# Kernel tuning notes

Hardware: AMD Instinct MI355X
Metric: run time of the kernel (lower is better)

## Reference

```python
import jax, jax.numpy as jnp
import numpy as np

N = 50000      # nodes
E = 800000     # edges
D_IN = 512
H = 256        # hidden_dim


def setup_inputs() -> dict:
    key = jax.random.key(0)
    ks = jax.random.split(key, 16)
    def w(k, shape):
        fan_in = shape[0]
        return (jax.random.normal(k, shape, jnp.float32) / np.sqrt(fan_in)).astype(jnp.float32)
    return {
        "x": jax.random.normal(ks[0], (N, D_IN), jnp.float32),
        "edge_index": jax.random.randint(ks[1], (2, E), 0, N),
        "W1": w(ks[2], (D_IN, H)),      "b1": jnp.zeros((H,), jnp.float32),
        "W2": w(ks[3], (H, H)),          "b2": jnp.zeros((H,), jnp.float32),
        "W3": w(ks[4], (H, H // 2)),     "b3": jnp.zeros((H // 2,), jnp.float32),
        "We": w(ks[5], (H // 2, 3)),     "be": jnp.zeros((3,), jnp.float32),
        "Wh": w(ks[6], (H // 2, 3)),     "bh": jnp.zeros((3,), jnp.float32),
        "Wg": w(ks[7], (H // 2, 3)),     "bg": jnp.zeros((3,), jnp.float32),
    }


def _gcn(h, W, b, src, dst, norm_edge, norm_self):
    # GCNConv: X' = D^{-1/2} (A + I) D^{-1/2} X W + b  (lin first, then aggregate)
    h = h @ W                                             # [N, out]
    msg = h[src] * norm_edge[:, None]                     # [E, out]
    agg = jax.ops.segment_sum(msg, dst, num_segments=N)   # neighbor sum
    agg = agg + h * norm_self[:, None]                    # self-loop term
    return agg + b


def reference(x, edge_index, W1, b1, W2, b2, W3, b3, We, be, Wh, bh, Wg, bg):
    src, dst = edge_index[0], edge_index[1]
    # degree of A + I (unit edge weights + self loop)
    deg = jax.ops.segment_sum(jnp.ones((E,), jnp.float32), dst, num_segments=N) + 1.0
    dinv = jax.lax.rsqrt(deg)
    norm_edge = dinv[src] * dinv[dst]   # [E]
    norm_self = dinv * dinv             # [N]

    h1 = jax.nn.relu(_gcn(x,  W1, b1, src, dst, norm_edge, norm_self))
    h2 = jax.nn.relu(_gcn(h1, W2, b2, src, dst, norm_edge, norm_self))
    h3 = jax.nn.relu(_gcn(h2, W3, b3, src, dst, norm_edge, norm_self))

    emp = h3 @ We + be
    hc  = h3 @ Wh + bh
    gro = h3 @ Wg + bg
    return jnp.concatenate([emp, hc, gro], axis=1)  # [N, 9]
```

## Files before the change

kernel.cpp:

```cpp
#include <hip/hip_runtime.h>

#define N_NODES 50000
#define N_EDGES 800000
#define MP 50048

typedef __attribute__((ext_vector_type(8))) short bf16x8;
typedef __attribute__((ext_vector_type(4))) float f32x4;
typedef _Float16 f16;
typedef __attribute__((ext_vector_type(4))) _Float16 half4;
typedef __attribute__((ext_vector_type(2))) _Float16 half2v;

__device__ __forceinline__ unsigned short f2bf(float f) {
    unsigned u = __float_as_uint(f);
    u += 0x7fffu + ((u >> 16) & 1u);
    return (unsigned short)(u >> 16);
}
__device__ __forceinline__ float bf2f(unsigned short h) {
    return __uint_as_float(((unsigned)h) << 16);
}


__global__ void hist_kernel(const int* __restrict__ dst, int* __restrict__ deg, int e) {
    int i = blockIdx.x * blockDim.x + threadIdx.x;
    if (i < e) atomicAdd(&deg[dst[i]], 1);
}

__global__ void dinv_kernel(const int* __restrict__ deg, float* __restrict__ dinv, int n) {
    int i = blockIdx.x * blockDim.x + threadIdx.x;
    if (i < n) dinv[i] = rsqrtf((float)deg[i] + 1.0f);
}

__global__ __launch_bounds__(1024) void scan_kernel(const int* __restrict__ counts,
                                                    int* __restrict__ row_start, int n) {
    __shared__ int wsum[16];
    __shared__ int carry_s;
    int tid = threadIdx.x, wid = tid >> 6, lane = tid & 63;
    if (tid == 0) carry_s = 0;
    __syncthreads();
    for (int base = 0; base < n; base += 1024) {
        int i = base + tid;
        int v = (i < n) ? counts[i] : 0;
        int s = v;
        #pragma unroll
        for (int off = 1; off < 64; off <<= 1) {
            int t = __shfl_up(s, off, 64);
            if (lane >= off) s += t;
        }
        if (lane == 63) wsum[wid] = s;
        __syncthreads();
        if (wid == 0) {
            int ws = (lane < 16) ? wsum[lane] : 0;
            #pragma unroll
            for (int off = 1; off < 16; off <<= 1) {
                int t = __shfl_up(ws, off, 64);
                if (lane >= off) ws += t;
            }
            if (lane < 16) wsum[lane] = ws;
        }
        __syncthreads();
        int carry = carry_s;
        if (i < n) row_start[i] = carry + ((wid == 0) ? 0 : wsum[wid - 1]) + s - v;
        int total = wsum[15];
        __syncthreads();
        if (tid == 0) carry_s = carry + total;
        __syncthreads();
    }
    if (tid == 0) row_start[n] = carry_s;
}

__global__ void scatter_kernel(const int* __restrict__ src, const int* __restrict__ dst,
                               const float* __restrict__ dinv,
                               const int* __restrict__ row_start, int* __restrict__ cursor,
                               int* __restrict__ csr_src, float* __restrict__ csr_w, int e) {
    int i = blockIdx.x * blockDim.x + threadIdx.x;
    if (i < e) {
        int d = dst[i], s = src[i];
        int p = atomicAdd(&cursor[d], 1);
        int idx = row_start[d] + p;
        csr_src[idx] = s;
        csr_w[idx] = dinv[s] * dinv[d];
    }
}


__global__ void wsplit_kernel(const float* __restrict__ W, unsigned short* __restrict__ Wh,
                              unsigned short* __restrict__ Wl, int K, int N) {
    int i = blockIdx.x * blockDim.x + threadIdx.x;
    if (i >= K * N) return;
    int k = i / N, n = i - k * N;
    float v = W[i];
    unsigned short h = f2bf(v);
    unsigned short l = f2bf(v - bf2f(h));
    Wh[(size_t)n * K + k] = h;
    Wl[(size_t)n * K + k] = l;
}


__global__ void xsplit_kernel(const float* __restrict__ x, unsigned short* __restrict__ Xh,
                              unsigned short* __restrict__ Xl, int total4) {
    int i = blockIdx.x * blockDim.x + threadIdx.x;
    if (i >= total4) return;
    float4 v = ((const float4*)x)[i];
    ushort4 h, l;
    h.x = f2bf(v.x); l.x = f2bf(v.x - bf2f(h.x));
    h.y = f2bf(v.y); l.y = f2bf(v.y - bf2f(h.y));
    h.z = f2bf(v.z); l.z = f2bf(v.z - bf2f(h.z));
    h.w = f2bf(v.w); l.w = f2bf(v.w - bf2f(h.w));
    ((ushort4*)Xh)[i] = h;
    ((ushort4*)Xl)[i] = l;
}


__global__ __launch_bounds__(256) void gemm_mfma(
    const unsigned short* __restrict__ Ah, const unsigned short* __restrict__ Al,
    const unsigned short* __restrict__ Bh, const unsigned short* __restrict__ Bl,
    f16* __restrict__ C, int M, int N, int K) {
    __shared__ __align__(16) char smem[32768];
    const int tid = threadIdx.x;
    const int wid = tid >> 6, lane = tid & 63;
    const int wr = wid >> 1, wc = wid & 1;
    const int rl = lane & 15, kg = lane >> 4;
    const int bn = blockIdx.x * 128;
    const int bm = blockIdx.y * 128;
    const size_t K2 = (size_t)K * 2;

    const int c0 = tid, r0 = c0 >> 2, g10 = c0 & 3;
    const int c1 = tid + 256, r1 = c1 >> 2, g11 = c1 & 3;
    const int g0 = (g10 - (r0 >> 1)) & 3;
    const int g1 = (g11 - (r1 >> 1)) & 3;

    const char* pAh0 = (const char*)Ah + (size_t)(bm + r0) * K2 + g0 * 16;
    const char* pAh1 = (const char*)Ah + (size_t)(bm + r1) * K2 + g1 * 16;
    const char* pAl0 = (const char*)Al + (size_t)(bm + r0) * K2 + g0 * 16;
    const char* pAl1 = (const char*)Al + (size_t)(bm + r1) * K2 + g1 * 16;
    const char* pBh0 = (const char*)Bh + (size_t)(bn + r0) * K2 + g0 * 16;
    const char* pBh1 = (const char*)Bh + (size_t)(bn + r1) * K2 + g1 * 16;
    const char* pBl0 = (const char*)Bl + (size_t)(bn + r0) * K2 + g0 * 16;
    const char* pBl1 = (const char*)Bl + (size_t)(bn + r1) * K2 + g1 * 16;

    const int lds_t0 = wid * 1024;
    const int lds_t1 = 4096 + wid * 1024;

    const int gp = (kg + (rl >> 1)) & 3;
    int offA[4], offB[4];
    #pragma unroll
    for (int m = 0; m < 4; ++m) offA[m] = (wr * 64 + m * 16 + rl) * 64 + gp * 16;
    #pragma unroll
    for (int n = 0; n < 4; ++n) offB[n] = (wc * 64 + n * 16 + rl) * 64 + gp * 16;

    f32x4 acc[4][4];
    #pragma unroll
    for (int m = 0; m < 4; ++m)
        #pragma unroll
        for (int n = 0; n < 4; ++n) acc[m][n] = (f32x4){0.f, 0.f, 0.f, 0.f};

#define GLOAD(g, loff)                                                                   \
    __builtin_amdgcn_global_load_lds((const __attribute__((address_space(1))) void*)(g), \
                                     (__attribute__((address_space(3))) void*)(smem + (loff)), \
                                     16, 0, 0)

    const int nk = K >> 5;
    for (int it = 0; it < nk; ++it) {
        const size_t kb = (size_t)it * 64;
        if (it) __syncthreads();
        GLOAD(pAh0 + kb, 0     + lds_t0);  GLOAD(pAh1 + kb, 0     + lds_t1);
        GLOAD(pAl0 + kb, 8192  + lds_t0);  GLOAD(pAl1 + kb, 8192  + lds_t1);
        GLOAD(pBh0 + kb, 16384 + lds_t0);  GLOAD(pBh1 + kb, 16384 + lds_t1);
        GLOAD(pBl0 + kb, 24576 + lds_t0);  GLOAD(pBl1 + kb, 24576 + lds_t1);
        __syncthreads();

        bf16x8 fah[4], fal[4], fbh[4], fbl[4];
        #pragma unroll
        for (int m = 0; m < 4; ++m) {
            fah[m] = *(const bf16x8*)(smem + offA[m]);
            fal[m] = *(const bf16x8*)(smem + 8192 + offA[m]);
        }
        #pragma unroll
        for (int n = 0; n < 4; ++n) {
            fbh[n] = *(const bf16x8*)(smem + 16384 + offB[n]);
            fbl[n] = *(const bf16x8*)(smem + 24576 + offB[n]);
        }
        #pragma unroll
        for (int m = 0; m < 4; ++m)
            #pragma unroll
            for (int n = 0; n < 4; ++n) {
                acc[m][n] = __builtin_amdgcn_mfma_f32_16x16x32_bf16(fah[m], fbh[n], acc[m][n], 0, 0, 0);
                acc[m][n] = __builtin_amdgcn_mfma_f32_16x16x32_bf16(fah[m], fbl[n], acc[m][n], 0, 0, 0);
                acc[m][n] = __builtin_amdgcn_mfma_f32_16x16x32_bf16(fal[m], fbh[n], acc[m][n], 0, 0, 0);
            }
    }
#undef GLOAD

    #pragma unroll
    for (int m = 0; m < 4; ++m) {
        const int rbase = bm + wr * 64 + m * 16 + kg * 4;
        #pragma unroll
        for (int n = 0; n < 4; ++n) {
            const int col = bn + wc * 64 + n * 16 + rl;
            f32x4 v = acc[m][n];
            #pragma unroll
            for (int j = 0; j < 4; ++j) {
                int row = rbase + j;
                if (row < M) C[(size_t)row * N + col] = (f16)v[j];
            }
        }
    }
}


__global__ __launch_bounds__(256) void aggregate4_kernel(
    const f16* __restrict__ hlin, const int* __restrict__ row_start,
    const int* __restrict__ csr_src, const float* __restrict__ csr_w,
    const float* __restrict__ dinv, const float* __restrict__ bias,
    unsigned short* __restrict__ oh, unsigned short* __restrict__ ol, int n) {
    constexpr int COLS = 256;
    int node = blockIdx.x * 4 + (threadIdx.x >> 6);
    int lane = threadIdx.x & 63;
    if (node >= n) return;
    int c0 = lane * 4;

    float acc[4];
    float dn = dinv[node];
    float ns = dn * dn;
    {
        half4 v = *(const half4*)(hlin + (size_t)node * COLS + c0);
        #pragma unroll
        for (int k = 0; k < 4; ++k) acc[k] = (float)v[k] * ns;
    }
    int beg = row_start[node], end = row_start[node + 1];
    int deg = end - beg;
    for (int base = 0; base < deg; base += 64) {
        int cnt = min(64, deg - base);
        int es = 0; float ew = 0.f;
        if (lane < cnt) {
            es = csr_src[beg + base + lane];
            ew = csr_w[beg + base + lane];
        }
        int i = 0;
        for (; i + 1 < cnt; i += 2) {
            int s0 = __shfl(es, i, 64);     float w0 = __shfl(ew, i, 64);
            int s1 = __shfl(es, i + 1, 64); float w1 = __shfl(ew, i + 1, 64);
            half4 v0 = *(const half4*)(hlin + (size_t)s0 * COLS + c0);
            half4 v1 = *(const half4*)(hlin + (size_t)s1 * COLS + c0);
            #pragma unroll
            for (int k = 0; k < 4; ++k) acc[k] = fmaf(w0, (float)v0[k], acc[k]);
            #pragma unroll
            for (int k = 0; k < 4; ++k) acc[k] = fmaf(w1, (float)v1[k], acc[k]);
        }
        if (i < cnt) {
            int s = __shfl(es, i, 64); float w = __shfl(ew, i, 64);
            half4 v = *(const half4*)(hlin + (size_t)s * COLS + c0);
            #pragma unroll
            for (int k = 0; k < 4; ++k) acc[k] = fmaf(w, (float)v[k], acc[k]);
        }
    }
    unsigned short hv[4], lv[4];
    #pragma unroll
    for (int v = 0; v < 4; ++v) {
        float val = fmaxf(acc[v] + bias[c0 + v], 0.0f);
        hv[v] = f2bf(val);
        lv[v] = f2bf(val - bf2f(hv[v]));
    }
    *(ushort4*)(oh + (size_t)node * COLS + c0) = make_ushort4(hv[0], hv[1], hv[2], hv[3]);
    *(ushort4*)(ol + (size_t)node * COLS + c0) = make_ushort4(lv[0], lv[1], lv[2], lv[3]);
}


__global__ __launch_bounds__(256) void agg_head_kernel(
    const f16* __restrict__ hlin, const int* __restrict__ row_start,
    const int* __restrict__ csr_src, const float* __restrict__ csr_w,
    const float* __restrict__ dinv, const float* __restrict__ bias,
    const float* __restrict__ We, const float* __restrict__ be,
    const float* __restrict__ Wh, const float* __restrict__ bh,
    const float* __restrict__ Wg, const float* __restrict__ bg,
    float* __restrict__ out, int n) {
    constexpr int COLS = 128;
    __shared__ float Ws[128][9];
    __shared__ float bs[9];
    int tid = threadIdx.x;
    for (int i = tid; i < 128 * 3; i += 256) {
        int r = i / 3, c = i % 3;
        Ws[r][c]     = We[i];
        Ws[r][c + 3] = Wh[i];
        Ws[r][c + 6] = Wg[i];
    }
    if (tid < 3) { bs[tid] = be[tid]; bs[tid + 3] = bh[tid]; bs[tid + 6] = bg[tid]; }
    __syncthreads();

    int node = blockIdx.x * 4 + (tid >> 6);
    int lane = tid & 63;
    if (node >= n) return;
    int c0 = lane * 2;

    float acc0, acc1;
    float dn = dinv[node];
    float ns = dn * dn;
    {
        half2v v = *(const half2v*)(hlin + (size_t)node * COLS + c0);
        acc0 = (float)v[0] * ns; acc1 = (float)v[1] * ns;
    }
    int beg = row_start[node], end = row_start[node + 1];
    int deg = end - beg;
    for (int base = 0; base < deg; base += 64) {
        int cnt = min(64, deg - base);
        int es = 0; float ew = 0.f;
        if (lane < cnt) {
            es = csr_src[beg + base + lane];
            ew = csr_w[beg + base + lane];
        }
        int i = 0;
        for (; i + 1 < cnt; i += 2) {
            int s0 = __shfl(es, i, 64);     float w0 = __shfl(ew, i, 64);
            int s1 = __shfl(es, i + 1, 64); float w1 = __shfl(ew, i + 1, 64);
            half2v v0 = *(const half2v*)(hlin + (size_t)s0 * COLS + c0);
            half2v v1 = *(const half2v*)(hlin + (size_t)s1 * COLS + c0);
            acc0 = fmaf(w0, (float)v0[0], acc0); acc1 = fmaf(w0, (float)v0[1], acc1);
            acc0 = fmaf(w1, (float)v1[0], acc0); acc1 = fmaf(w1, (float)v1[1], acc1);
        }
        if (i < cnt) {
            int s = __shfl(es, i, 64); float w = __shfl(ew, i, 64);
            half2v v = *(const half2v*)(hlin + (size_t)s * COLS + c0);
            acc0 = fmaf(w, (float)v[0], acc0); acc1 = fmaf(w, (float)v[1], acc1);
        }
    }
    float h0 = fmaxf(acc0 + bias[c0], 0.0f);
    float h1 = fmaxf(acc1 + bias[c0 + 1], 0.0f);
    #pragma unroll
    for (int c = 0; c < 9; ++c) {
        float p = h0 * Ws[c0][c] + h1 * Ws[c0 + 1][c];
        #pragma unroll
        for (int m = 1; m < 64; m <<= 1) p += __shfl_xor(p, m, 64);
        if (lane == 0) out[(size_t)node * 9 + c] = p + bs[c];
    }
}


extern "C" void kernel_launch(void* const* d_in, const int* in_sizes, int n_in,
                              void* d_out, int out_size, void* d_ws, size_t ws_size,
                              hipStream_t stream) {
    const float* x  = (const float*)d_in[0];
    const int*   ei = (const int*)d_in[1];
    const float* W1 = (const float*)d_in[2];
    const float* b1 = (const float*)d_in[3];
    const float* W2 = (const float*)d_in[4];
    const float* b2 = (const float*)d_in[5];
    const float* W3 = (const float*)d_in[6];
    const float* b3 = (const float*)d_in[7];
    const float* We = (const float*)d_in[8];
    const float* be = (const float*)d_in[9];
    const float* Wh = (const float*)d_in[10];
    const float* bh = (const float*)d_in[11];
    const float* Wg = (const float*)d_in[12];
    const float* bg = (const float*)d_in[13];
    float* out = (float*)d_out;

    const int* src = ei;
    const int* dst = ei + N_EDGES;

    char* ws = (char*)d_ws;
    size_t off = 0;
    auto alloc = [&](size_t bytes) {
        void* p = ws + off;
        off = (off + bytes + 255) & ~(size_t)255;
        return p;
    };
    int*   deg       = (int*)alloc(N_NODES * 4);
    float* dinv      = (float*)alloc(N_NODES * 4);
    int*   row_start = (int*)alloc((N_NODES + 1) * 4);
    int*   cursor    = (int*)alloc(N_NODES * 4);
    int*   csr_src   = (int*)alloc(N_EDGES * 4);
    float* csr_w     = (float*)alloc(N_EDGES * 4);
    unsigned short* Xh = (unsigned short*)alloc((size_t)MP * 512 * 2);
    unsigned short* Xl = (unsigned short*)alloc((size_t)MP * 512 * 2);
    f16* Cbuf = (f16*)alloc((size_t)MP * 256 * 2);
    unsigned short* W1h = (unsigned short*)alloc(512 * 256 * 2);
    unsigned short* W1l = (unsigned short*)alloc(512 * 256 * 2);
    unsigned short* W2h = (unsigned short*)alloc(256 * 256 * 2);
    unsigned short* W2l = (unsigned short*)alloc(256 * 256 * 2);
    unsigned short* W3h = (unsigned short*)alloc(256 * 128 * 2);
    unsigned short* W3l = (unsigned short*)alloc(256 * 128 * 2);

    unsigned short* Hh = Xh;
    unsigned short* Hl = Xl;

    hipMemsetAsync(deg, 0, N_NODES * 4, stream);
    hipMemsetAsync(cursor, 0, N_NODES * 4, stream);

    hist_kernel<<<(N_EDGES + 255) / 256, 256, 0, stream>>>(dst, deg, N_EDGES);
    dinv_kernel<<<(N_NODES + 255) / 256, 256, 0, stream>>>(deg, dinv, N_NODES);
    scan_kernel<<<1, 1024, 0, stream>>>(deg, row_start, N_NODES);
    scatter_kernel<<<(N_EDGES + 255) / 256, 256, 0, stream>>>(src, dst, dinv, row_start, cursor,
                                                              csr_src, csr_w, N_EDGES);

    wsplit_kernel<<<(512 * 256 + 255) / 256, 256, 0, stream>>>(W1, W1h, W1l, 512, 256);
    wsplit_kernel<<<(256 * 256 + 255) / 256, 256, 0, stream>>>(W2, W2h, W2l, 256, 256);
    wsplit_kernel<<<(256 * 128 + 255) / 256, 256, 0, stream>>>(W3, W3h, W3l, 256, 128);
    xsplit_kernel<<<(N_NODES * 512 / 4 + 255) / 256, 256, 0, stream>>>(x, Xh, Xl, N_NODES * 512 / 4);

    dim3 blk(256);
    gemm_mfma<<<dim3(2, MP / 128), blk, 0, stream>>>(Xh, Xl, W1h, W1l, Cbuf, N_NODES, 256, 512);
    aggregate4_kernel<<<(N_NODES + 3) / 4, blk, 0, stream>>>(
        Cbuf, row_start, csr_src, csr_w, dinv, b1, Hh, Hl, N_NODES);
    gemm_mfma<<<dim3(2, MP / 128), blk, 0, stream>>>(Hh, Hl, W2h, W2l, Cbuf, N_NODES, 256, 256);
    aggregate4_kernel<<<(N_NODES + 3) / 4, blk, 0, stream>>>(
        Cbuf, row_start, csr_src, csr_w, dinv, b2, Hh, Hl, N_NODES);
    gemm_mfma<<<dim3(1, MP / 128), blk, 0, stream>>>(Hh, Hl, W3h, W3l, Cbuf, N_NODES, 128, 256);
    agg_head_kernel<<<(N_NODES + 3) / 4, blk, 0, stream>>>(
        Cbuf, row_start, csr_src, csr_w, dinv, b3, We, be, Wh, bh, Wg, bg, out, N_NODES);
}
```

Baseline: 626.8 us.

## Pack CSR src/weight pairs, unroll gather loops, merge weight split and memsets

Stores each edge's source index and weight together as one int2, so the aggregation kernels make one 8-byte uniform load per edge. The per-wave ballot/shuffle edge staging is replaced by 16- and 4-wide unrolled gathers that keep many row loads in flight per wave. The three weight-split kernels and the two memsets are merged into a single kernel, which cuts launch count. The head kernel drops its shared-memory weight staging and block barrier, keeps weights in registers, and interleaves the nine reductions. The unrolled loops raise register pressure, which may lower occupancy.

```diff
diff --git a/kernel.cpp b/kernel.cpp
--- a/kernel.cpp
+++ b/kernel.cpp
@@ -71,28 +71,36 @@
 __global__ void scatter_kernel(const int* __restrict__ src, const int* __restrict__ dst,
                                const float* __restrict__ dinv,
                                const int* __restrict__ row_start, int* __restrict__ cursor,
-                               int* __restrict__ csr_src, float* __restrict__ csr_w, int e) {
+                               int2* __restrict__ csr_sw, int e) {
     int i = blockIdx.x * blockDim.x + threadIdx.x;
     if (i < e) {
         int d = dst[i], s = src[i];
         int p = atomicAdd(&cursor[d], 1);
         int idx = row_start[d] + p;
-        csr_src[idx] = s;
-        csr_w[idx] = dinv[s] * dinv[d];
-    }
-}
-
-
-__global__ void wsplit_kernel(const float* __restrict__ W, unsigned short* __restrict__ Wh,
-                              unsigned short* __restrict__ Wl, int K, int N) {
-    int i = blockIdx.x * blockDim.x + threadIdx.x;
-    if (i >= K * N) return;
+        csr_sw[idx] = make_int2(s, __float_as_int(dinv[s] * dinv[d]));
+    }
+}
+
+
+__global__ void wsplit3_kernel(const float* __restrict__ W1, unsigned short* __restrict__ W1h,
+                               unsigned short* __restrict__ W1l,
+                               const float* __restrict__ W2, unsigned short* __restrict__ W2h,
+                               unsigned short* __restrict__ W2l,
+                               const float* __restrict__ W3, unsigned short* __restrict__ W3h,
+                               unsigned short* __restrict__ W3l,
+                               int* __restrict__ deg, int* __restrict__ cursor) {
+    int gi = blockIdx.x * blockDim.x + threadIdx.x;
+    if (gi < N_NODES) { deg[gi] = 0; cursor[gi] = 0; }
+    const float* W; unsigned short *Wh_, *Wl_; int K, N, i = gi;
+    if (i < 131072)      { W = W1; Wh_ = W1h; Wl_ = W1l; K = 512; N = 256; }
+    else if (i < 196608) { i -= 131072; W = W2; Wh_ = W2h; Wl_ = W2l; K = 256; N = 256; }
+    else                 { i -= 196608; W = W3; Wh_ = W3h; Wl_ = W3l; K = 256; N = 128; }
     int k = i / N, n = i - k * N;
     float v = W[i];
     unsigned short h = f2bf(v);
     unsigned short l = f2bf(v - bf2f(h));
-    Wh[(size_t)n * K + k] = h;
-    Wl[(size_t)n * K + k] = l;
+    Wh_[(size_t)n * K + k] = h;
+    Wl_[(size_t)n * K + k] = l;
 }
 
 
@@ -210,7 +218,7 @@
 
 __global__ __launch_bounds__(256) void aggregate4_kernel(
     const f16* __restrict__ hlin, const int* __restrict__ row_start,
-    const int* __restrict__ csr_src, const float* __restrict__ csr_w,
+    const int2* __restrict__ csr_sw,
     const float* __restrict__ dinv, const float* __restrict__ bias,
     unsigned short* __restrict__ oh, unsigned short* __restrict__ ol, int n) {
     constexpr int COLS = 256;
@@ -227,32 +235,44 @@
         #pragma unroll
         for (int k = 0; k < 4; ++k) acc[k] = (float)v[k] * ns;
     }
-    int beg = row_start[node], end = row_start[node + 1];
-    int deg = end - beg;
-    for (int base = 0; base < deg; base += 64) {
-        int cnt = min(64, deg - base);
-        int es = 0; float ew = 0.f;
-        if (lane < cnt) {
-            es = csr_src[beg + base + lane];
-            ew = csr_w[beg + base + lane];
-        }
-        int i = 0;
-        for (; i + 1 < cnt; i += 2) {
-            int s0 = __shfl(es, i, 64);     float w0 = __shfl(ew, i, 64);
-            int s1 = __shfl(es, i + 1, 64); float w1 = __shfl(ew, i + 1, 64);
-            half4 v0 = *(const half4*)(hlin + (size_t)s0 * COLS + c0);
-            half4 v1 = *(const half4*)(hlin + (size_t)s1 * COLS + c0);
+    int beg = __builtin_amdgcn_readfirstlane(row_start[node]);
+    int end = __builtin_amdgcn_readfirstlane(row_start[node + 1]);
+
+    int j = beg;
+    for (; j + 16 <= end; j += 16) {
+        int2 e[16]; half4 vv[16];
+        #pragma unroll
+        for (int t = 0; t < 16; ++t) e[t] = csr_sw[j + t];
+        #pragma unroll
+        for (int t = 0; t < 16; ++t)
+            vv[t] = *(const half4*)(hlin + (size_t)e[t].x * COLS + c0);
+        #pragma unroll
+        for (int t = 0; t < 16; ++t) {
+            float w = __int_as_float(e[t].y);
             #pragma unroll
-            for (int k = 0; k < 4; ++k) acc[k] = fmaf(w0, (float)v0[k], acc[k]);
+            for (int k = 0; k < 4; ++k) acc[k] = fmaf(w, (float)vv[t][k], acc[k]);
+        }
+    }
+    for (; j + 4 <= end; j += 4) {
+        int2 e[4]; half4 vv[4];
+        #pragma unroll
+        for (int t = 0; t < 4; ++t) e[t] = csr_sw[j + t];
+        #pragma unroll
+        for (int t = 0; t < 4; ++t)
+            vv[t] = *(const half4*)(hlin + (size_t)e[t].x * COLS + c0);
+        #pragma unroll
+        for (int t = 0; t < 4; ++t) {
+            float w = __int_as_float(e[t].y);
             #pragma unroll
-            for (int k = 0; k < 4; ++k) acc[k] = fmaf(w1, (float)v1[k], acc[k]);
-        }
-        if (i < cnt) {
-            int s = __shfl(es, i, 64); float w = __shfl(ew, i, 64);
-            half4 v = *(const half4*)(hlin + (size_t)s * COLS + c0);
-            #pragma unroll
-            for (int k = 0; k < 4; ++k) acc[k] = fmaf(w, (float)v[k], acc[k]);
-        }
+            for (int k = 0; k < 4; ++k) acc[k] = fmaf(w, (float)vv[t][k], acc[k]);
+        }
+    }
+    for (; j < end; ++j) {
+        int2 e = csr_sw[j];
+        half4 v = *(const half4*)(hlin + (size_t)e.x * COLS + c0);
+        float w = __int_as_float(e.y);
+        #pragma unroll
+        for (int k = 0; k < 4; ++k) acc[k] = fmaf(w, (float)v[k], acc[k]);
     }
     unsigned short hv[4], lv[4];
     #pragma unroll
@@ -268,29 +288,25 @@
 
 __global__ __launch_bounds__(256) void agg_head_kernel(
     const f16* __restrict__ hlin, const int* __restrict__ row_start,
-    const int* __restrict__ csr_src, const float* __restrict__ csr_w,
+    const int2* __restrict__ csr_sw,
     const float* __restrict__ dinv, const float* __restrict__ bias,
     const float* __restrict__ We, const float* __restrict__ be,
     const float* __restrict__ Wh, const float* __restrict__ bh,
     const float* __restrict__ Wg, const float* __restrict__ bg,
     float* __restrict__ out, int n) {
     constexpr int COLS = 128;
-    __shared__ float Ws[128][9];
-    __shared__ float bs[9];
-    int tid = threadIdx.x;
-    for (int i = tid; i < 128 * 3; i += 256) {
-        int r = i / 3, c = i % 3;
-        Ws[r][c]     = We[i];
-        Ws[r][c + 3] = Wh[i];
-        Ws[r][c + 6] = Wg[i];
-    }
-    if (tid < 3) { bs[tid] = be[tid]; bs[tid + 3] = bh[tid]; bs[tid + 6] = bg[tid]; }
-    __syncthreads();
-
-    int node = blockIdx.x * 4 + (tid >> 6);
-    int lane = tid & 63;
+    int node = blockIdx.x * 4 + (threadIdx.x >> 6);
+    int lane = threadIdx.x & 63;
     if (node >= n) return;
     int c0 = lane * 2;
+
+    float w0r[9], w1r[9];
+    #pragma unroll
+    for (int c = 0; c < 3; ++c) {
+        w0r[c]     = We[c0 * 3 + c];       w1r[c]     = We[(c0 + 1) * 3 + c];
+        w0r[c + 3] = Wh[c0 * 3 + c];       w1r[c + 3] = Wh[(c0 + 1) * 3 + c];
+        w0r[c + 6] = Wg[c0 * 3 + c];       w1r[c + 6] = Wg[(c0 + 1) * 3 + c];
+    }
 
     float acc0, acc1;
     float dn = dinv[node];
@@ -299,38 +315,61 @@
         half2v v = *(const half2v*)(hlin + (size_t)node * COLS + c0);
         acc0 = (float)v[0] * ns; acc1 = (float)v[1] * ns;
     }
-    int beg = row_start[node], end = row_start[node + 1];
-    int deg = end - beg;
-    for (int base = 0; base < deg; base += 64) {
-        int cnt = min(64, deg - base);
-        int es = 0; float ew = 0.f;
-        if (lane < cnt) {
-            es = csr_src[beg + base + lane];
-            ew = csr_w[beg + base + lane];
-        }
-        int i = 0;
-        for (; i + 1 < cnt; i += 2) {
-            int s0 = __shfl(es, i, 64);     float w0 = __shfl(ew, i, 64);
-            int s1 = __shfl(es, i + 1, 64); float w1 = __shfl(ew, i + 1, 64);
-            half2v v0 = *(const half2v*)(hlin + (size_t)s0 * COLS + c0);
-            half2v v1 = *(const half2v*)(hlin + (size_t)s1 * COLS + c0);
-            acc0 = fmaf(w0, (float)v0[0], acc0); acc1 = fmaf(w0, (float)v0[1], acc1);
-            acc0 = fmaf(w1, (float)v1[0], acc0); acc1 = fmaf(w1, (float)v1[1], acc1);
-        }
-        if (i < cnt) {
-            int s = __shfl(es, i, 64); float w = __shfl(ew, i, 64);
-            half2v v = *(const half2v*)(hlin + (size_t)s * COLS + c0);
-            acc0 = fmaf(w, (float)v[0], acc0); acc1 = fmaf(w, (float)v[1], acc1);
-        }
+    int beg = __builtin_amdgcn_readfirstlane(row_start[node]);
+    int end = __builtin_amdgcn_readfirstlane(row_start[node + 1]);
+
+    int j = beg;
+    for (; j + 16 <= end; j += 16) {
+        int2 e[16]; half2v vv[16];
+        #pragma unroll
+        for (int t = 0; t < 16; ++t) e[t] = csr_sw[j + t];
+        #pragma unroll
+        for (int t = 0; t < 16; ++t)
+            vv[t] = *(const half2v*)(hlin + (size_t)e[t].x * COLS + c0);
+        #pragma unroll
+        for (int t = 0; t < 16; ++t) {
+            float w = __int_as_float(e[t].y);
+            acc0 = fmaf(w, (float)vv[t][0], acc0);
+            acc1 = fmaf(w, (float)vv[t][1], acc1);
+        }
+    }
+    for (; j + 4 <= end; j += 4) {
+        int2 e[4]; half2v vv[4];
+        #pragma unroll
+        for (int t = 0; t < 4; ++t) e[t] = csr_sw[j + t];
+        #pragma unroll
+        for (int t = 0; t < 4; ++t)
+            vv[t] = *(const half2v*)(hlin + (size_t)e[t].x * COLS + c0);
+        #pragma unroll
+        for (int t = 0; t < 4; ++t) {
+            float w = __int_as_float(e[t].y);
+            acc0 = fmaf(w, (float)vv[t][0], acc0);
+            acc1 = fmaf(w, (float)vv[t][1], acc1);
+        }
+    }
+    for (; j < end; ++j) {
+        int2 e = csr_sw[j];
+        half2v v = *(const half2v*)(hlin + (size_t)e.x * COLS + c0);
+        float w = __int_as_float(e.y);
+        acc0 = fmaf(w, (float)v[0], acc0);
+        acc1 = fmaf(w, (float)v[1], acc1);
     }
     float h0 = fmaxf(acc0 + bias[c0], 0.0f);
     float h1 = fmaxf(acc1 + bias[c0 + 1], 0.0f);
-    #pragma unroll
-    for (int c = 0; c < 9; ++c) {
-        float p = h0 * Ws[c0][c] + h1 * Ws[c0 + 1][c];
-        #pragma unroll
-        for (int m = 1; m < 64; m <<= 1) p += __shfl_xor(p, m, 64);
-        if (lane == 0) out[(size_t)node * 9 + c] = p + bs[c];
+
+    float p[9];
+    #pragma unroll
+    for (int c = 0; c < 9; ++c) p[c] = h0 * w0r[c] + h1 * w1r[c];
+    #pragma unroll
+    for (int m = 1; m < 64; m <<= 1)
+        #pragma unroll
+        for (int c = 0; c < 9; ++c) p[c] += __shfl_xor(p[c], m, 64);
+    if (lane == 0) {
+        #pragma unroll
+        for (int c = 0; c < 9; ++c) {
+            float b = (c < 3) ? be[c] : (c < 6) ? bh[c - 3] : bg[c - 6];
+            out[(size_t)node * 9 + c] = p[c] + b;
+        }
     }
 }
 
@@ -368,8 +407,7 @@
     float* dinv      = (float*)alloc(N_NODES * 4);
     int*   row_start = (int*)alloc((N_NODES + 1) * 4);
     int*   cursor    = (int*)alloc(N_NODES * 4);
-    int*   csr_src   = (int*)alloc(N_EDGES * 4);
-    float* csr_w     = (float*)alloc(N_EDGES * 4);
+    int2*  csr_sw    = (int2*)alloc((size_t)N_EDGES * 8);
     unsigned short* Xh = (unsigned short*)alloc((size_t)MP * 512 * 2);
     unsigned short* Xl = (unsigned short*)alloc((size_t)MP * 512 * 2);
     f16* Cbuf = (f16*)alloc((size_t)MP * 256 * 2);
@@ -383,28 +421,24 @@
     unsigned short* Hh = Xh;
     unsigned short* Hl = Xl;
 
-    hipMemsetAsync(deg, 0, N_NODES * 4, stream);
-    hipMemsetAsync(cursor, 0, N_NODES * 4, stream);
+    wsplit3_kernel<<<896, 256, 0, stream>>>(W1, W1h, W1l, W2, W2h, W2l, W3, W3h, W3l,
+                                            deg, cursor);
+    xsplit_kernel<<<(N_NODES * 512 / 4 + 255) / 256, 256, 0, stream>>>(x, Xh, Xl, N_NODES * 512 / 4);
 
     hist_kernel<<<(N_EDGES + 255) / 256, 256, 0, stream>>>(dst, deg, N_EDGES);
     dinv_kernel<<<(N_NODES + 255) / 256, 256, 0, stream>>>(deg, dinv, N_NODES);
     scan_kernel<<<1, 1024, 0, stream>>>(deg, row_start, N_NODES);
     scatter_kernel<<<(N_EDGES + 255) / 256, 256, 0, stream>>>(src, dst, dinv, row_start, cursor,
-                                                              csr_src, csr_w, N_EDGES);
-
-    wsplit_kernel<<<(512 * 256 + 255) / 256, 256, 0, stream>>>(W1, W1h, W1l, 512, 256);
-    wsplit_kernel<<<(256 * 256 + 255) / 256, 256, 0, stream>>>(W2, W2h, W2l, 256, 256);
-    wsplit_kernel<<<(256 * 128 + 255) / 256, 256, 0, stream>>>(W3, W3h, W3l, 256, 128);
-    xsplit_kernel<<<(N_NODES * 512 / 4 + 255) / 256, 256, 0, stream>>>(x, Xh, Xl, N_NODES * 512 / 4);
+                                                              csr_sw, N_EDGES);
 
     dim3 blk(256);
     gemm_mfma<<<dim3(2, MP / 128), blk, 0, stream>>>(Xh, Xl, W1h, W1l, Cbuf, N_NODES, 256, 512);
     aggregate4_kernel<<<(N_NODES + 3) / 4, blk, 0, stream>>>(
-        Cbuf, row_start, csr_src, csr_w, dinv, b1, Hh, Hl, N_NODES);
+        Cbuf, row_start, csr_sw, dinv, b1, Hh, Hl, N_NODES);
     gemm_mfma<<<dim3(2, MP / 128), blk, 0, stream>>>(Hh, Hl, W2h, W2l, Cbuf, N_NODES, 256, 256);
     aggregate4_kernel<<<(N_NODES + 3) / 4, blk, 0, stream>>>(
-        Cbuf, row_start, csr_src, csr_w, dinv, b2, Hh, Hl, N_NODES);
+        Cbuf, row_start, csr_sw, dinv, b2, Hh, Hl, N_NODES);
     gemm_mfma<<<dim3(1, MP / 128), blk, 0, stream>>>(Hh, Hl, W3h, W3l, Cbuf, N_NODES, 128, 256);
     agg_head_kernel<<<(N_NODES + 3) / 4, blk, 0, stream>>>(
-        Cbuf, row_start, csr_src, csr_w, dinv, b3, We, be, Wh, bh, Wg, bg, out, N_NODES);
-}
+        Cbuf, row_start, csr_sw, dinv, b3, We, be, Wh, bh, Wg, bg, out, N_NODES);
+}
```

New measurement: 576.5 us. -8.0%, faster.
